# Performance work log

Hardware: AMD Instinct MI355X
Metric: run time of the kernel (lower is better)

The kernel has to match this reference:

```python
import jax, jax.numpy as jnp
from jax import lax
import numpy as np

K = 2000      # self.k: entries kept per sample
T_SC = 3      # number of IHT iterations
DN = ('NCHW', 'OIHW', 'NCHW')


def keep_k_largest(X, k):
    # Per-sample hard threshold: keep the k largest-magnitude entries of the
    # flattened [C,H,W] activations, zero the rest (exactly k kept, as in argsort).
    B = X.shape[0]
    flat = X.reshape(B, -1)                                # [B, N]
    _, idx = lax.top_k(jnp.abs(flat), k)                   # [B, k]
    vals = jnp.take_along_axis(flat, idx, axis=1)          # [B, k]
    out = jnp.zeros_like(flat).at[jnp.arange(B)[:, None], idx].set(vals)
    return out.reshape(X.shape)


def _D_apply(X, W_D):
    # ConvTranspose2d(numb_atom -> dp_channels), stride 1, no padding:
    # full correlation with the spatially flipped, io-swapped kernel.
    kh, kw = W_D.shape[2], W_D.shape[3]
    Wt = jnp.flip(jnp.transpose(W_D, (1, 0, 2, 3)), (2, 3))  # [dp, atoms, kh, kw]
    return lax.conv_general_dilated(X, Wt, (1, 1),
                                    [(kh - 1, kh - 1), (kw - 1, kw - 1)],
                                    dimension_numbers=DN)


def _Dt_apply(Z, W_D):
    # Conv2d(dp_channels -> numb_atom) VALID; D_trans.weight = D.weight.permute(0,1,3,2)
    Wt = jnp.transpose(W_D, (0, 1, 3, 2))                  # [atoms, dp, kh, kw]
    return lax.conv_general_dilated(Z, Wt, (1, 1), 'VALID', dimension_numbers=DN)


def setup_inputs() -> dict:
    key = jax.random.key(0)
    k1, k2, k3 = jax.random.split(key, 3)
    Y = jax.random.normal(k1, (32, 3, 64, 64), jnp.float32)
    X0 = jax.random.normal(k2, (32, 128, 57, 57), jnp.float32)   # random init X in forward
    W_D = jax.random.normal(k3, (128, 3, 8, 8), jnp.float32) * 0.05
    return {"Y": Y, "X0": X0, "W_D": W_D}


def reference(Y, X0, W_D):
    # HT_arg = X - D_trans(D(X) - Y); then T_SC hard-threshold iterations.
    HT_arg = X0 - _Dt_apply(_D_apply(X0, W_D) - Y, W_D)
    X = HT_arg
    for i in range(T_SC):
        X = keep_k_largest(HT_arg, K)
        if i < T_SC - 1:  # final HT_arg update in the original is unused
            HT_arg = X - _Dt_apply(_D_apply(X, W_D) - Y, W_D)
    return X
```

## Files before the change

### kernel.cpp

```cpp
#include <hip/hip_runtime.h>

#define BATCH 32
#define ATOMS 128
#define CCH 3
#define XH 57
#define XW 57
#define OHH 64
#define OWW 64
#define KSEL 2000
#define PIX (XH*XW)
#define NPS (ATOMS*PIX)
#define NTOT (BATCH*NPS)
#define RPS (CCH*OHH*OWW)
#define RTOT (BATCH*RPS)
#define CANDCAP 32768
#define NW 24576
#define NWC 32768
#define LCAP 6144
#define ZWORDS (32*2048 + 32)

__global__ __launch_bounds__(256) void prep_k(const float* __restrict__ Wg,
    double* __restrict__ WDd, float* __restrict__ Wt2f,
    float* __restrict__ Wcand, const float* __restrict__ Y,
    double* __restrict__ Rd, unsigned* __restrict__ zbuf) {
  int e = blockIdx.x * 256 + threadIdx.x;
  if (e < NW) {
    {
      int kw = e & 7; int t = e >> 3; int c = t % 3; t /= 3; int kh = t & 7; int a = t >> 3;
      WDd[e] = (double)Wg[(a*3 + c)*64 + kh*8 + kw];
    }
    {
      int a = e & 127; int t = e >> 7; int j = t & 7; int i = (t >> 3) & 7; int c = t >> 6;
      Wt2f[e] = Wg[(a*3 + c)*64 + j*8 + i];
    }
  }
  if (e < NWC) {
    int a = e >> 8, r = e & 255;
    float v = 0.0f;
    if (r < 192) {
      int c = r >> 6, ii = (r >> 3) & 7, jj = r & 7;
      v = Wg[(a*3 + c)*64 + jj*8 + ii];
    }
    Wcand[e] = v;
  }
  if (e < RTOT) Rd[e] = -(double)Y[e];
  if (e < ZWORDS) zbuf[e] = 0;
}

__global__ __launch_bounds__(256) void convD_k(const float* __restrict__ X,
    const double* __restrict__ WDd, double* __restrict__ Rd) {
  __shared__ double Xs[4][11][72];
  int p = blockIdx.x;
  int lg = (p & 7) * 256 + (p >> 3);
  int b = lg >> 6; int rem = lg & 63;
  int band = rem >> 2, quarter = rem & 3;
  int row0 = band * 4;
  int a_base = quarter * 32;
  int tid = threadIdx.x;
  int ox = tid & 63;
  int wv = __builtin_amdgcn_readfirstlane(tid >> 6);
  const float* Xb = X + (size_t)b * NPS;

  double acc[4][3];
#pragma unroll
  for (int ty = 0; ty < 4; ++ty)
#pragma unroll
    for (int c = 0; c < 3; ++c) acc[ty][c] = 0.0;

  for (int ch = 0; ch < 8; ++ch) {
    __syncthreads();
    for (int e = tid; e < 4 * 11 * 72; e += 256) {
      int ai = e / 792; int rem2 = e - ai * 792;
      int r = rem2 / 72; int ss = rem2 - r * 72;
      int gy = row0 - 7 + r;
      int xcol = ss - 7;
      int a = a_base + ch * 4 + ai;
      float v = 0.0f;
      if ((unsigned)xcol < (unsigned)XW && (unsigned)gy < (unsigned)XH)
        v = Xb[a * PIX + gy * XW + xcol];
      Xs[ai][r][ss] = (double)v;
    }
    __syncthreads();
    {
      int a = a_base + ch * 4 + wv;
      const double* Wa = WDd + a * 192;
#pragma unroll
      for (int r = 0; r < 11; ++r) {
        int gy = row0 - 7 + r;
        if ((unsigned)gy >= (unsigned)XH) continue;
        double xd[8];
#pragma unroll
        for (int t = 0; t < 8; ++t) xd[t] = Xs[wv][r][ox + t];
#pragma unroll
        for (int ty = 0; ty < 4; ++ty) {
          int kh = ty + 7 - r;
          if ((unsigned)kh < 8u) {
            const double* Wk = Wa + kh * 24;
#pragma unroll
            for (int kw = 0; kw < 8; ++kw) {
              acc[ty][0] = fma(xd[7 - kw], Wk[kw],      acc[ty][0]);
              acc[ty][1] = fma(xd[7 - kw], Wk[8 + kw],  acc[ty][1]);
              acc[ty][2] = fma(xd[7 - kw], Wk[16 + kw], acc[ty][2]);
            }
          }
        }
      }
    }
  }
#pragma unroll
  for (int ty = 0; ty < 4; ++ty) {
    int oy = row0 + ty;
#pragma unroll
    for (int c = 0; c < 3; ++c)
      atomicAdd(&Rd[((size_t)(b * CCH + c) << 12) + (oy << 6) + ox], acc[ty][c]);
  }
}

__global__ __launch_bounds__(256) void convD_sparse_k(const float* __restrict__ Wg,
    const int* __restrict__ nzidx, const float* __restrict__ nzval,
    const float* __restrict__ Y, float* __restrict__ R) {
  __shared__ double accd[512];
  __shared__ float Wf[8192];
  __shared__ int   li[KSEL];
  __shared__ float lv[KSEL];
  int p = blockIdx.x;
  int lg = (p & 7) * 96 + (p >> 3);
  int s = lg / 24; int r = lg % 24; int c = r >> 3; int band = r & 7;
  int row0 = band * 8;
  int tid = threadIdx.x;
  for (int e = tid; e < 512; e += 256) accd[e] = 0.0;
  for (int e = tid; e < 8192; e += 256) {
    int a = e >> 6, k2 = e & 63;
    Wf[e] = Wg[(a * 3 + c) * 64 + k2];
  }
  for (int e = tid; e < KSEL; e += 256) {
    li[e] = nzidx[s * KSEL + e];
    lv[e] = nzval[s * KSEL + e];
  }
  __syncthreads();
  int slot = tid >> 3, kw = tid & 7;
  for (int e = slot; e < KSEL; e += 32) {
    int idx = li[e];
    int a = (int)((unsigned)idx / 3249u);
    int pp = idx - a * 3249;
    int y = (int)((unsigned)pp / 57u);
    int x = pp - y * 57;
    int dy = y - row0;
    if (dy < -7 || dy > 7) continue;
    double val = (double)lv[e];
    const float* wp = Wf + (a << 6) + kw;
#pragma unroll
    for (int kh = 0; kh < 8; ++kh) {
      int rr = dy + kh;
      if ((unsigned)rr < 8u)
        __hip_atomic_fetch_add(&accd[(rr << 6) + x + kw],
                               val * (double)wp[kh << 3],
                               __ATOMIC_RELAXED, __HIP_MEMORY_SCOPE_WORKGROUP);
    }
  }
  __syncthreads();
  const float* Yb = Y + (((size_t)(s * CCH + c)) << 12) + (row0 << 6);
  float* Rb = R + (((size_t)(s * CCH + c)) << 12) + (row0 << 6);
  for (int e = tid; e < 512; e += 256)
    Rb[e] = (float)(accd[e] - (double)Yb[e]);
}

template <typename TR>
__global__ __launch_bounds__(256) void convDt_k(const TR* __restrict__ R,
    const float* __restrict__ Wt2f, const float* __restrict__ Xprev,
    float* __restrict__ HT, unsigned* __restrict__ g1) {
  __shared__ float Rl[3][15][72];
  __shared__ unsigned hh[1024];
  int p = blockIdx.x;
  int lg = (p & 7) * 512 + (p >> 3);
  int b = lg >> 7; int rem = lg & 127; int ag = rem >> 3; int by = rem & 7;
  int row0 = by * 8;
  int a0 = ag * 8;
  int tid = threadIdx.x;
  for (int e = tid; e < 1024; e += 256) hh[e] = 0;
  for (int e = tid; e < 3 * 15 * 72; e += 256) {
    int c = e / (15 * 72); int r2 = e - c * (15 * 72);
    int rr = r2 / 72; int cc = r2 - rr * 72;
    int gr = row0 + rr;
    float v = 0.0f;
    if (cc < OWW && gr < OHH)
      v = (float)R[((size_t)(b * CCH + c) << 12) + (gr << 6) + cc];
    Rl[c][rr][cc] = v;
  }
  __syncthreads();
  int x = tid & 63, yg = tid >> 6;
  int yb = yg * 2;
  float acc[8][2];
#pragma unroll
  for (int aa = 0; aa < 8; ++aa) { acc[aa][0] = 0.0f; acc[aa][1] = 0.0f; }

#pragma unroll 1
  for (int c = 0; c < 3; ++c) {
#pragma unroll 1
    for (int j = 0; j < 8; ++j) {
      float rw[9];
#pragma unroll
      for (int r = 0; r < 9; ++r) rw[r] = Rl[c][yb + r][x + j];
#pragma unroll
      for (int i = 0; i < 8; ++i) {
        const float* wp = Wt2f + ((c * 8 + i) * 8 + j) * 128 + a0;
#pragma unroll
        for (int aa = 0; aa < 8; ++aa) {
          float w = wp[aa];
          acc[aa][0] = fmaf(rw[i + 0], w, acc[aa][0]);
          acc[aa][1] = fmaf(rw[i + 1], w, acc[aa][1]);
        }
      }
    }
  }
  if (x < XW) {
#pragma unroll
    for (int ty = 0; ty < 2; ++ty) {
      int yy = row0 + yb + ty;
      if (yy < XH) {
#pragma unroll
        for (int aa = 0; aa < 8; ++aa) {
          size_t xo = (size_t)(b * ATOMS + a0 + aa) * PIX + yy * XW + x;
          float fv = Xprev[xo] - acc[aa][ty];
          HT[xo] = fv;
          unsigned u = __float_as_uint(fv) & 0x7fffffffu;
          unsigned bin = u >> 20;
          atomicAdd(&hh[bin >> 1], 1u << ((bin & 1) << 4));
        }
      }
    }
  }
  __syncthreads();
  unsigned* gp = g1 + (size_t)b * 2048;
  for (int e = tid; e < 1024; e += 256) {
    unsigned v = hh[e];
    unsigned lo = v & 0xffffu, hi = v >> 16;
    if (lo) atomicAdd(&gp[2 * e], lo);
    if (hi) atomicAdd(&gp[2 * e + 1], hi);
  }
}

template <typename TR>
__global__ __launch_bounds__(256) void histwrite_k(const float* __restrict__ HT,
    const unsigned* __restrict__ g1, const TR* __restrict__ R,
    const float* __restrict__ Wcand, const float* Xp,
    int* __restrict__ cand, int* __restrict__ candcnt,
    float* __restrict__ candval, float* Xo) {
  __shared__ unsigned part[256];
  __shared__ int lidx[LCAP];
  __shared__ int lcnt, lbase, b1_sh;
  int tid = threadIdx.x;
  int s = blockIdx.x >> 5;
  int chunk = blockIdx.x & 31;
  const unsigned* hg1 = g1 + (size_t)s * 2048;
  unsigned psum = 0;
#pragma unroll
  for (int e = 0; e < 8; ++e) psum += hg1[tid * 8 + e];
  part[tid] = psum;
  if (tid == 0) lcnt = 0;
  __syncthreads();
  if (tid == 0) {
    int Kv = KSEL;
    unsigned cumBefore = 0;
    int bsel = 0;
    for (int q = 255; q >= 0; --q) {
      unsigned ps = part[q];
      if ((int)(cumBefore + ps) >= Kv) {
        for (int e = q * 8 + 7;; --e) {
          unsigned c2 = cumBefore + hg1[e];
          if ((int)c2 >= Kv) { bsel = e; break; }
          cumBefore = c2;
        }
        break;
      }
      cumBefore += ps;
    }
    b1_sh = bsel;
  }
  __syncthreads();
  unsigned blo = (unsigned)(b1_sh >= 2 ? b1_sh - 2 : 0);
  size_t sbase = (size_t)s * NPS;
  const uint4* U4 = (const uint4*)(HT + sbase);
  float4* X4 = (float4*)(Xo + sbase);
  for (int i4 = chunk * 256 + tid; i4 < NPS / 4; i4 += 32 * 256) {
    uint4 v = U4[i4];
    unsigned uu[4] = {v.x, v.y, v.z, v.w};
    int m = 0;
#pragma unroll
    for (int t = 0; t < 4; ++t) {
      unsigned u = uu[t] & 0x7fffffffu;
      if ((u >> 20) >= blo) {
        m |= 1 << t;
        int pos = atomicAdd(&lcnt, 1);
        if (pos < LCAP) lidx[pos] = i4 * 4 + t;
      }
    }
    if (m == 0) {
      X4[i4] = make_float4(0.0f, 0.0f, 0.0f, 0.0f);
    } else {
#pragma unroll
      for (int t = 0; t < 4; ++t)
        if (!(m & (1 << t))) Xo[sbase + i4 * 4 + t] = 0.0f;
    }
  }
  __syncthreads();
  if (tid == 0) {
    int nn = lcnt < LCAP ? lcnt : LCAP;
    lbase = atomicAdd(&candcnt[s], nn);
  }
  __syncthreads();
  int nn = lcnt < LCAP ? lcnt : LCAP;
  const TR* Rb = R + ((size_t)(s * 3) << 12);
  for (int e = tid; e < nn; e += 256) {
    int i = lidx[e];
    int g = lbase + e;
    int a = (int)((unsigned)i / 3249u);
    int p = i - a * 3249;
    int y = (int)((unsigned)p / 57u);
    int x = p - y * 57;
    double xprev = (double)Xp[sbase + i];
    const float* wa = Wcand + (a << 8);
    double acc = 0.0;
    for (int c = 0; c < 3; ++c) {
#pragma unroll
      for (int ii = 0; ii < 8; ++ii) {
        const TR* rrow = Rb + (c << 12) + ((y + ii) << 6) + x;
        const float* wrow = wa + (c * 8 + ii) * 8;
#pragma unroll
        for (int jj = 0; jj < 8; ++jj)
          acc = fma((double)rrow[jj], (double)wrow[jj], acc);
      }
    }
    float cf = (float)(xprev - acc);
    if (g < CANDCAP) {
      cand[s * CANDCAP + g] = i;
      candval[s * CANDCAP + g] = cf;
    }
  }
}

__global__ __launch_bounds__(256) void pass3_k(const int* __restrict__ cand,
    int* __restrict__ candcnt, const float* __restrict__ candval,
    unsigned* __restrict__ g1, float* __restrict__ Xo,
    int* __restrict__ nzidx, float* __restrict__ nzval, int emit) {
  int s = blockIdx.x;
  __shared__ unsigned h[2048];
  __shared__ unsigned part[256];
  __shared__ int eqidx[1024];
  __shared__ int kidx[2048];
  __shared__ float kval[2048];
  __shared__ int eqn, kcnt;
  __shared__ unsigned tau_sh;
  __shared__ int k3_sh, cutoff_sh, b1_sh, k1_sh, b2_sh, k2_sh;
  int t = threadIdx.x;
  int n = candcnt[s];
  if (n > CANDCAP) n = CANDCAP;
  const int* cs = cand + s * CANDCAP;
  const float* cv = candval + s * CANDCAP;
  for (int e = t; e < 2048; e += 256) h[e] = 0;
  if (t == 0) { eqn = 0; kcnt = 0; }
  __syncthreads();
  for (int e = t; e < n; e += 256) {
    unsigned u = __float_as_uint(cv[e]) & 0x7fffffffu;
    atomicAdd(&h[u >> 20], 1u);
  }
  __syncthreads();
  unsigned s1 = 0;
#pragma unroll
  for (int e = 0; e < 8; ++e) s1 += h[t * 8 + e];
  part[t] = s1;
  __syncthreads();
  if (t == 0) {
    int Kv = KSEL;
    unsigned cumBefore = 0;
    int bsel = 0;
    for (int q = 255; q >= 0; --q) {
      unsigned ps = part[q];
      if ((int)(cumBefore + ps) >= Kv) {
        for (int e = q * 8 + 7;; --e) {
          unsigned c2 = cumBefore + h[e];
          if ((int)c2 >= Kv) { bsel = e; break; }
          cumBefore = c2;
        }
        break;
      }
      cumBefore += ps;
    }
    b1_sh = bsel;
    k1_sh = KSEL - (int)cumBefore;
  }
  __syncthreads();
  unsigned b1x = (unsigned)b1_sh;
  for (int e = t; e < 1024; e += 256) h[e] = 0;
  __syncthreads();
  for (int e = t; e < n; e += 256) {
    unsigned u = __float_as_uint(cv[e]) & 0x7fffffffu;
    if ((u >> 20) == b1x) atomicAdd(&h[(u >> 10) & 1023], 1u);
  }
  __syncthreads();
  part[t] = h[t * 4] + h[t * 4 + 1] + h[t * 4 + 2] + h[t * 4 + 3];
  __syncthreads();
  if (t == 0) {
    int Kv = k1_sh;
    unsigned cumBefore = 0;
    int bsel = 0;
    for (int q = 255; q >= 0; --q) {
      unsigned ps = part[q];
      if ((int)(cumBefore + ps) >= Kv) {
        for (int e = q * 4 + 3;; --e) {
          unsigned c2 = cumBefore + h[e];
          if ((int)c2 >= Kv) { bsel = e; break; }
          cumBefore = c2;
        }
        break;
      }
      cumBefore += ps;
    }
    b2_sh = bsel;
    k2_sh = Kv - (int)cumBefore;
  }
  __syncthreads();
  for (int e = t; e < 1024; e += 256) h[e] = 0;
  __syncthreads();
  unsigned pre21 = (b1x << 10) | (unsigned)b2_sh;
  for (int e = t; e < n; e += 256) {
    unsigned u = __float_as_uint(cv[e]) & 0x7fffffffu;
    if ((u >> 10) == pre21) atomicAdd(&h[u & 1023], 1u);
  }
  __syncthreads();
  if (t == 0) {
    int Kv = k2_sh;
    unsigned cumBefore = 0;
    int b3 = 0;
    for (int e = 1023; e >= 0; --e) {
      unsigned c2 = cumBefore + h[e];
      if ((int)c2 >= Kv) { b3 = e; break; }
      cumBefore = c2;
    }
    tau_sh = (pre21 << 10) | (unsigned)b3;
    k3_sh = Kv - (int)cumBefore;
  }
  __syncthreads();
  unsigned tau = tau_sh;
  for (int e = t; e < n; e += 256) {
    unsigned u = __float_as_uint(cv[e]) & 0x7fffffffu;
    if (u == tau) {
      int pos = atomicAdd(&eqn, 1);
      if (pos < 1024) eqidx[pos] = cs[e];
    }
  }
  __syncthreads();
  if (t == 0) {
    int m = eqn < 1024 ? eqn : 1024;
    int k3 = k3_sh;
    int cutoff;
    if (k3 >= m) {
      cutoff = 0x7fffffff;
    } else {
      int last = -1;
      for (int r = 0; r < k3; ++r) {
        int mn = 0x7fffffff;
        for (int q = 0; q < m; ++q) {
          int v = eqidx[q];
          if (v > last && v < mn) mn = v;
        }
        last = mn;
      }
      cutoff = last;
    }
    cutoff_sh = cutoff;
  }
  __syncthreads();
  int co = cutoff_sh;
  float* Xs = Xo + (size_t)s * NPS;
  for (int e = t; e < n; e += 256) {
    int i = cs[e];
    float cf = cv[e];
    unsigned u = __float_as_uint(cf) & 0x7fffffffu;
    bool keep = (u > tau) || (u == tau && i <= co);
    Xs[i] = keep ? cf : 0.0f;
    if (keep && emit) {
      int pos = atomicAdd(&kcnt, 1);
      if (pos < 2048) { kidx[pos] = i; kval[pos] = cf; }
    }
  }
  __syncthreads();
  if (emit) {
    int kn = kcnt < KSEL ? kcnt : KSEL;
    for (int e = t; e < kn; e += 256) {
      nzidx[s * KSEL + e] = kidx[e];
      nzval[s * KSEL + e] = kval[e];
    }
  }
  unsigned* hg1 = g1 + (size_t)s * 2048;
  for (int e = t; e < 2048; e += 256) hg1[e] = 0;
  if (t == 0) candcnt[s] = 0;
}

extern "C" void kernel_launch(void* const* d_in, const int* in_sizes, int n_in,
                              void* d_out, int out_size, void* d_ws, size_t ws_size,
                              hipStream_t stream) {
  const float* Y  = (const float*)d_in[0];
  const float* X0 = (const float*)d_in[1];
  const float* Wg = (const float*)d_in[2];
  float* Xout = (float*)d_out;

  double* WDd  = (double*)d_ws;
  float* Wt2f  = (float*)(WDd + NW);
  float* Wcand = Wt2f + NW;
  float* HT   = Wcand + NWC;
  float* Rbuf = HT + NTOT;
  double* Rd  = (double*)(Rbuf + RTOT);
  unsigned* g1 = (unsigned*)(Rd + RTOT);
  int* candcnt = (int*)(g1 + 32 * 2048);
  int* cand = candcnt + 32;
  float* candval = (float*)(cand + 32 * CANDCAP);
  int* nzidx = (int*)(candval + 32 * CANDCAP);
  float* nzval = (float*)(nzidx + 32 * KSEL);

  prep_k<<<dim3((RTOT + 255) / 256), dim3(256), 0, stream>>>(
      Wg, WDd, Wt2f, Wcand, Y, Rd, g1);

  for (int it = 0; it < 3; ++it) {
    if (it == 0) {
      convD_k<<<dim3(2048), dim3(256), 0, stream>>>(X0, WDd, Rd);
      convDt_k<double><<<dim3(4096), dim3(256), 0, stream>>>(Rd, Wt2f, X0, HT, g1);
      histwrite_k<double><<<dim3(BATCH * 32), dim3(256), 0, stream>>>(
          HT, g1, Rd, Wcand, X0, cand, candcnt, candval, Xout);
    } else {
      convD_sparse_k<<<dim3(BATCH * CCH * 8), dim3(256), 0, stream>>>(
          Wg, nzidx, nzval, Y, Rbuf);
      convDt_k<float><<<dim3(4096), dim3(256), 0, stream>>>(Rbuf, Wt2f,
          (const float*)Xout, HT, g1);
      histwrite_k<float><<<dim3(BATCH * 32), dim3(256), 0, stream>>>(
          HT, g1, Rbuf, Wcand, (const float*)Xout, cand, candcnt, candval, Xout);
    }
    int emit = (it < 2) ? 1 : 0;
    pass3_k<<<dim3(BATCH), dim3(256), 0, stream>>>(
        cand, candcnt, candval, g1, Xout, nzidx, nzval, emit);
  }
}
```

Measured before the change: 942.4 us.

## Fuse top-k selection into histwrite via last-block pattern and reconstruct sparse X in-place

```diff
diff --git a/kernel.cpp b/kernel.cpp
--- a/kernel.cpp
+++ b/kernel.cpp
@@ -17,7 +17,7 @@
 #define NW 24576
 #define NWC 32768
 #define LCAP 6144
-#define ZWORDS (32*2048 + 32)
+#define ZWORDS (32*2048 + 64)
 
 __global__ __launch_bounds__(256) void prep_k(const float* __restrict__ Wg,
     double* __restrict__ WDd, float* __restrict__ Wt2f,
@@ -165,10 +165,11 @@
     Rb[e] = (float)(accd[e] - (double)Yb[e]);
 }
 
-template <typename TR>
+template <typename TR, bool RECON>
 __global__ __launch_bounds__(256) void convDt_k(const TR* __restrict__ R,
-    const float* __restrict__ Wt2f, const float* __restrict__ Xprev,
-    float* __restrict__ HT, unsigned* __restrict__ g1) {
+    const float* __restrict__ Wt2f, const float* Xsrc, float* HT,
+    const unsigned* __restrict__ tauArr, const int* __restrict__ cutArr,
+    unsigned* __restrict__ g1) {
   __shared__ float Rl[3][15][72];
   __shared__ unsigned hh[1024];
   int p = blockIdx.x;
@@ -177,6 +178,8 @@
   int row0 = by * 8;
   int a0 = ag * 8;
   int tid = threadIdx.x;
+  unsigned tt = 0; int co = 0;
+  if constexpr (RECON) { tt = tauArr[b]; co = cutArr[b]; }
   for (int e = tid; e < 1024; e += 256) hh[e] = 0;
   for (int e = tid; e < 3 * 15 * 72; e += 256) {
     int c = e / (15 * 72); int r2 = e - c * (15 * 72);
@@ -221,7 +224,16 @@
 #pragma unroll
         for (int aa = 0; aa < 8; ++aa) {
           size_t xo = (size_t)(b * ATOMS + a0 + aa) * PIX + yy * XW + x;
-          float fv = Xprev[xo] - acc[aa][ty];
+          float xprev;
+          if constexpr (RECON) {
+            float hp = HT[xo];
+            unsigned hu = __float_as_uint(hp) & 0x7fffffffu;
+            int il = (a0 + aa) * PIX + yy * XW + x;
+            xprev = (hu > tt || (hu == tt && il <= co)) ? hp : 0.0f;
+          } else {
+            xprev = Xsrc[xo];
+          }
+          float fv = xprev - acc[aa][ty];
           HT[xo] = fv;
           unsigned u = __float_as_uint(fv) & 0x7fffffffu;
           unsigned bin = u >> 20;
@@ -240,19 +252,28 @@
   }
 }
 
-template <typename TR>
-__global__ __launch_bounds__(256) void histwrite_k(const float* __restrict__ HT,
-    const unsigned* __restrict__ g1, const TR* __restrict__ R,
-    const float* __restrict__ Wcand, const float* Xp,
+union ShU {
+  int lidx[LCAP];
+  struct { int hidx[4096]; float hval[4096]; } hs;
+  struct { unsigned h[2048]; int eqidx[1024];
+           int kidx[2048]; float kval[2048]; } p3;
+};
+
+template <typename TR, bool RECON, bool FINAL>
+__global__ __launch_bounds__(256) void histwrite_k(float* HT,
+    unsigned* __restrict__ g1, const TR* __restrict__ R,
+    const float* __restrict__ Wcand, const float* __restrict__ Xp,
     int* __restrict__ cand, int* __restrict__ candcnt,
-    float* __restrict__ candval, float* Xo) {
+    float* __restrict__ candval, unsigned* __restrict__ done,
+    float* __restrict__ Xo, int* __restrict__ nzidx, float* __restrict__ nzval,
+    unsigned* __restrict__ tauArr, int* __restrict__ cutArr) {
+  __shared__ ShU u;
   __shared__ unsigned part[256];
-  __shared__ int lidx[LCAP];
-  __shared__ int lcnt, lbase, b1_sh;
+  __shared__ int lcnt, lbase, b1_sh, islast;
   int tid = threadIdx.x;
   int s = blockIdx.x >> 5;
   int chunk = blockIdx.x & 31;
-  const unsigned* hg1 = g1 + (size_t)s * 2048;
+  unsigned* hg1 = g1 + (size_t)s * 2048;
   unsigned psum = 0;
 #pragma unroll
   for (int e = 0; e < 8; ++e) psum += hg1[tid * 8 + e];
@@ -281,26 +302,27 @@
   unsigned blo = (unsigned)(b1_sh >= 2 ? b1_sh - 2 : 0);
   size_t sbase = (size_t)s * NPS;
   const uint4* U4 = (const uint4*)(HT + sbase);
-  float4* X4 = (float4*)(Xo + sbase);
   for (int i4 = chunk * 256 + tid; i4 < NPS / 4; i4 += 32 * 256) {
     uint4 v = U4[i4];
     unsigned uu[4] = {v.x, v.y, v.z, v.w};
     int m = 0;
 #pragma unroll
     for (int t = 0; t < 4; ++t) {
-      unsigned u = uu[t] & 0x7fffffffu;
-      if ((u >> 20) >= blo) {
+      unsigned uv = uu[t] & 0x7fffffffu;
+      if ((uv >> 20) >= blo) {
         m |= 1 << t;
         int pos = atomicAdd(&lcnt, 1);
-        if (pos < LCAP) lidx[pos] = i4 * 4 + t;
-      }
-    }
-    if (m == 0) {
-      X4[i4] = make_float4(0.0f, 0.0f, 0.0f, 0.0f);
-    } else {
-#pragma unroll
-      for (int t = 0; t < 4; ++t)
-        if (!(m & (1 << t))) Xo[sbase + i4 * 4 + t] = 0.0f;
+        if (pos < LCAP) u.lidx[pos] = i4 * 4 + t;
+      }
+    }
+    if constexpr (FINAL) {
+      if (m == 0) {
+        ((float4*)(Xo + sbase))[i4] = make_float4(0.0f, 0.0f, 0.0f, 0.0f);
+      } else {
+#pragma unroll
+        for (int t = 0; t < 4; ++t)
+          if (!(m & (1 << t))) Xo[sbase + i4 * 4 + t] = 0.0f;
+      }
     }
   }
   __syncthreads();
@@ -312,13 +334,13 @@
   int nn = lcnt < LCAP ? lcnt : LCAP;
   const TR* Rb = R + ((size_t)(s * 3) << 12);
   for (int e = tid; e < nn; e += 256) {
-    int i = lidx[e];
+    int i = u.lidx[e];
     int g = lbase + e;
     int a = (int)((unsigned)i / 3249u);
     int p = i - a * 3249;
     int y = (int)((unsigned)p / 57u);
     int x = p - y * 57;
-    double xprev = (double)Xp[sbase + i];
+    double xprev = RECON ? 0.0 : (double)Xp[sbase + i];
     const float* wa = Wcand + (a << 8);
     double acc = 0.0;
     for (int c = 0; c < 3; ++c) {
@@ -337,37 +359,61 @@
       candval[s * CANDCAP + g] = cf;
     }
   }
-}
-
-__global__ __launch_bounds__(256) void pass3_k(const int* __restrict__ cand,
-    int* __restrict__ candcnt, const float* __restrict__ candval,
-    unsigned* __restrict__ g1, float* __restrict__ Xo,
-    int* __restrict__ nzidx, float* __restrict__ nzval, int emit) {
-  int s = blockIdx.x;
-  __shared__ unsigned h[2048];
-  __shared__ unsigned part[256];
-  __shared__ int eqidx[1024];
-  __shared__ int kidx[2048];
-  __shared__ float kval[2048];
-  __shared__ int eqn, kcnt;
-  __shared__ unsigned tau_sh;
-  __shared__ int k3_sh, cutoff_sh, b1_sh, k1_sh, b2_sh, k2_sh;
-  int t = threadIdx.x;
+  __threadfence();
+  __syncthreads();
+  if (tid == 0) {
+    unsigned prev = atomicAdd(&done[s], 1u);
+    islast = (prev == 31);
+  }
+  __syncthreads();
+  if (!islast) return;
+  __threadfence();
+
+  int t = tid;
   int n = candcnt[s];
   if (n > CANDCAP) n = CANDCAP;
   const int* cs = cand + s * CANDCAP;
-  const float* cv = candval + s * CANDCAP;
-  for (int e = t; e < 2048; e += 256) h[e] = 0;
+  float* cvp = candval + s * CANDCAP;
+  if constexpr (RECON) {
+    for (int e = t; e < 4096; e += 256) u.hs.hidx[e] = -1;
+    __syncthreads();
+    for (int e = t; e < KSEL; e += 256) {
+      int idx = nzidx[s * KSEL + e];
+      float v = nzval[s * KSEL + e];
+      int slot = idx & 4095;
+      while (true) {
+        int old = atomicCAS(&u.hs.hidx[slot], -1, idx);
+        if (old == -1) { u.hs.hval[slot] = v; break; }
+        slot = (slot + 1) & 4095;
+      }
+    }
+    __syncthreads();
+    for (int e = t; e < n; e += 256) {
+      int i = cs[e];
+      int slot = i & 4095;
+      while (true) {
+        int h = u.hs.hidx[slot];
+        if (h == i) { cvp[e] += u.hs.hval[slot]; break; }
+        if (h == -1) break;
+        slot = (slot + 1) & 4095;
+      }
+    }
+    __syncthreads();
+  }
+  __shared__ int eqn, kcnt;
+  __shared__ unsigned tau_sh;
+  __shared__ int k3_sh, cutoff_sh, b1x_sh, k1_sh, b2_sh, k2_sh;
+  for (int e = t; e < 2048; e += 256) u.p3.h[e] = 0;
   if (t == 0) { eqn = 0; kcnt = 0; }
   __syncthreads();
   for (int e = t; e < n; e += 256) {
-    unsigned u = __float_as_uint(cv[e]) & 0x7fffffffu;
-    atomicAdd(&h[u >> 20], 1u);
+    unsigned uv = __float_as_uint(cvp[e]) & 0x7fffffffu;
+    atomicAdd(&u.p3.h[uv >> 20], 1u);
   }
   __syncthreads();
   unsigned s1 = 0;
 #pragma unroll
-  for (int e = 0; e < 8; ++e) s1 += h[t * 8 + e];
+  for (int e = 0; e < 8; ++e) s1 += u.p3.h[t * 8 + e];
   part[t] = s1;
   __syncthreads();
   if (t == 0) {
@@ -378,7 +424,7 @@
       unsigned ps = part[q];
       if ((int)(cumBefore + ps) >= Kv) {
         for (int e = q * 8 + 7;; --e) {
-          unsigned c2 = cumBefore + h[e];
+          unsigned c2 = cumBefore + u.p3.h[e];
           if ((int)c2 >= Kv) { bsel = e; break; }
           cumBefore = c2;
         }
@@ -386,19 +432,19 @@
       }
       cumBefore += ps;
     }
-    b1_sh = bsel;
+    b1x_sh = bsel;
     k1_sh = KSEL - (int)cumBefore;
   }
   __syncthreads();
-  unsigned b1x = (unsigned)b1_sh;
-  for (int e = t; e < 1024; e += 256) h[e] = 0;
+  unsigned b1x = (unsigned)b1x_sh;
+  for (int e = t; e < 1024; e += 256) u.p3.h[e] = 0;
   __syncthreads();
   for (int e = t; e < n; e += 256) {
-    unsigned u = __float_as_uint(cv[e]) & 0x7fffffffu;
-    if ((u >> 20) == b1x) atomicAdd(&h[(u >> 10) & 1023], 1u);
-  }
-  __syncthreads();
-  part[t] = h[t * 4] + h[t * 4 + 1] + h[t * 4 + 2] + h[t * 4 + 3];
+    unsigned uv = __float_as_uint(cvp[e]) & 0x7fffffffu;
+    if ((uv >> 20) == b1x) atomicAdd(&u.p3.h[(uv >> 10) & 1023], 1u);
+  }
+  __syncthreads();
+  part[t] = u.p3.h[t*4] + u.p3.h[t*4+1] + u.p3.h[t*4+2] + u.p3.h[t*4+3];
   __syncthreads();
   if (t == 0) {
     int Kv = k1_sh;
@@ -408,7 +454,7 @@
       unsigned ps = part[q];
       if ((int)(cumBefore + ps) >= Kv) {
         for (int e = q * 4 + 3;; --e) {
-          unsigned c2 = cumBefore + h[e];
+          unsigned c2 = cumBefore + u.p3.h[e];
           if ((int)c2 >= Kv) { bsel = e; break; }
           cumBefore = c2;
         }
@@ -420,12 +466,12 @@
     k2_sh = Kv - (int)cumBefore;
   }
   __syncthreads();
-  for (int e = t; e < 1024; e += 256) h[e] = 0;
+  for (int e = t; e < 1024; e += 256) u.p3.h[e] = 0;
   __syncthreads();
   unsigned pre21 = (b1x << 10) | (unsigned)b2_sh;
   for (int e = t; e < n; e += 256) {
-    unsigned u = __float_as_uint(cv[e]) & 0x7fffffffu;
-    if ((u >> 10) == pre21) atomicAdd(&h[u & 1023], 1u);
+    unsigned uv = __float_as_uint(cvp[e]) & 0x7fffffffu;
+    if ((uv >> 10) == pre21) atomicAdd(&u.p3.h[uv & 1023], 1u);
   }
   __syncthreads();
   if (t == 0) {
@@ -433,7 +479,7 @@
     unsigned cumBefore = 0;
     int b3 = 0;
     for (int e = 1023; e >= 0; --e) {
-      unsigned c2 = cumBefore + h[e];
+      unsigned c2 = cumBefore + u.p3.h[e];
       if ((int)c2 >= Kv) { b3 = e; break; }
       cumBefore = c2;
     }
@@ -443,10 +489,10 @@
   __syncthreads();
   unsigned tau = tau_sh;
   for (int e = t; e < n; e += 256) {
-    unsigned u = __float_as_uint(cv[e]) & 0x7fffffffu;
-    if (u == tau) {
+    unsigned uv = __float_as_uint(cvp[e]) & 0x7fffffffu;
+    if (uv == tau) {
       int pos = atomicAdd(&eqn, 1);
-      if (pos < 1024) eqidx[pos] = cs[e];
+      if (pos < 1024) u.p3.eqidx[pos] = cs[e];
     }
   }
   __syncthreads();
@@ -461,7 +507,7 @@
       for (int r = 0; r < k3; ++r) {
         int mn = 0x7fffffff;
         for (int q = 0; q < m; ++q) {
-          int v = eqidx[q];
+          int v = u.p3.eqidx[q];
           if (v > last && v < mn) mn = v;
         }
         last = mn;
@@ -472,29 +518,32 @@
   }
   __syncthreads();
   int co = cutoff_sh;
-  float* Xs = Xo + (size_t)s * NPS;
   for (int e = t; e < n; e += 256) {
     int i = cs[e];
-    float cf = cv[e];
-    unsigned u = __float_as_uint(cf) & 0x7fffffffu;
-    bool keep = (u > tau) || (u == tau && i <= co);
-    Xs[i] = keep ? cf : 0.0f;
-    if (keep && emit) {
-      int pos = atomicAdd(&kcnt, 1);
-      if (pos < 2048) { kidx[pos] = i; kval[pos] = cf; }
-    }
-  }
-  __syncthreads();
-  if (emit) {
+    float cf = cvp[e];
+    unsigned uv = __float_as_uint(cf) & 0x7fffffffu;
+    bool keep = (uv > tau) || (uv == tau && i <= co);
+    if constexpr (FINAL) {
+      Xo[sbase + i] = keep ? cf : 0.0f;
+    } else {
+      HT[sbase + i] = cf;
+      if (keep) {
+        int pos = atomicAdd(&kcnt, 1);
+        if (pos < 2048) { u.p3.kidx[pos] = i; u.p3.kval[pos] = cf; }
+      }
+    }
+  }
+  __syncthreads();
+  if constexpr (!FINAL) {
     int kn = kcnt < KSEL ? kcnt : KSEL;
     for (int e = t; e < kn; e += 256) {
-      nzidx[s * KSEL + e] = kidx[e];
-      nzval[s * KSEL + e] = kval[e];
-    }
-  }
-  unsigned* hg1 = g1 + (size_t)s * 2048;
+      nzidx[s * KSEL + e] = u.p3.kidx[e];
+      nzval[s * KSEL + e] = u.p3.kval[e];
+    }
+    if (t == 0) { tauArr[s] = tau; cutArr[s] = co; }
+  }
   for (int e = t; e < 2048; e += 256) hg1[e] = 0;
-  if (t == 0) candcnt[s] = 0;
+  if (t == 0) { candcnt[s] = 0; done[s] = 0; }
 }
 
 extern "C" void kernel_launch(void* const* d_in, const int* in_sizes, int n_in,
@@ -513,10 +562,13 @@
   double* Rd  = (double*)(Rbuf + RTOT);
   unsigned* g1 = (unsigned*)(Rd + RTOT);
   int* candcnt = (int*)(g1 + 32 * 2048);
-  int* cand = candcnt + 32;
+  unsigned* done = (unsigned*)(candcnt + 32);
+  int* cand = (int*)(done + 32);
   float* candval = (float*)(cand + 32 * CANDCAP);
   int* nzidx = (int*)(candval + 32 * CANDCAP);
   float* nzval = (float*)(nzidx + 32 * KSEL);
+  unsigned* tauArr = (unsigned*)(nzval + 32 * KSEL);
+  int* cutArr = (int*)(tauArr + 32);
 
   prep_k<<<dim3((RTOT + 255) / 256), dim3(256), 0, stream>>>(
       Wg, WDd, Wt2f, Wcand, Y, Rd, g1);
@@ -524,19 +576,25 @@
   for (int it = 0; it < 3; ++it) {
     if (it == 0) {
       convD_k<<<dim3(2048), dim3(256), 0, stream>>>(X0, WDd, Rd);
-      convDt_k<double><<<dim3(4096), dim3(256), 0, stream>>>(Rd, Wt2f, X0, HT, g1);
-      histwrite_k<double><<<dim3(BATCH * 32), dim3(256), 0, stream>>>(
-          HT, g1, Rd, Wcand, X0, cand, candcnt, candval, Xout);
+      convDt_k<double, false><<<dim3(4096), dim3(256), 0, stream>>>(
+          Rd, Wt2f, X0, HT, tauArr, cutArr, g1);
+      histwrite_k<double, false, false><<<dim3(BATCH * 32), dim3(256), 0, stream>>>(
+          HT, g1, Rd, Wcand, X0, cand, candcnt, candval, done,
+          Xout, nzidx, nzval, tauArr, cutArr);
     } else {
       convD_sparse_k<<<dim3(BATCH * CCH * 8), dim3(256), 0, stream>>>(
           Wg, nzidx, nzval, Y, Rbuf);
-      convDt_k<float><<<dim3(4096), dim3(256), 0, stream>>>(Rbuf, Wt2f,
-          (const float*)Xout, HT, g1);
-      histwrite_k<float><<<dim3(BATCH * 32), dim3(256), 0, stream>>>(
-          HT, g1, Rbuf, Wcand, (const float*)Xout, cand, candcnt, candval, Xout);
-    }
-    int emit = (it < 2) ? 1 : 0;
-    pass3_k<<<dim3(BATCH), dim3(256), 0, stream>>>(
-        cand, candcnt, candval, g1, Xout, nzidx, nzval, emit);
+      convDt_k<float, true><<<dim3(4096), dim3(256), 0, stream>>>(
+          Rbuf, Wt2f, HT, HT, tauArr, cutArr, g1);
+      if (it == 1) {
+        histwrite_k<float, true, false><<<dim3(BATCH * 32), dim3(256), 0, stream>>>(
+            HT, g1, Rbuf, Wcand, X0, cand, candcnt, candval, done,
+            Xout, nzidx, nzval, tauArr, cutArr);
+      } else {
+        histwrite_k<float, true, true><<<dim3(BATCH * 32), dim3(256), 0, stream>>>(
+            HT, g1, Rbuf, Wcand, X0, cand, candcnt, candval, done,
+            Xout, nzidx, nzval, tauArr, cutArr);
+      }
+    }
   }
 }
```

New measurement: 1.327 ms. 1.41x slower.
